# Optimization experiments

Measured on AMD Instinct MI355X. Metric: run time of the kernel, lower is better.

Reference implementation:

```python
import jax, jax.numpy as jnp
import numpy as np

N = 50000
F = 128
E = 800000
HOP = 3
ALPHA = 0.2  # leaky relu slope


def setup_inputs() -> dict:
    key = jax.random.key(0)
    ks = jax.random.split(key, 6)
    x = jax.random.normal(ks[0], (N, F), dtype=jnp.float32)
    h0 = jax.random.normal(ks[1], (N, F), dtype=jnp.float32)
    edge_index = jax.random.randint(ks[2], (2, E), 0, N, dtype=jnp.int32)
    edge_weight = jax.random.uniform(ks[3], (E,), dtype=jnp.float32)
    # xavier-uniform-ish params
    lim_w = float(np.sqrt(6.0 / (F + F)))
    W_att = jax.random.uniform(ks[4], (F, F), dtype=jnp.float32, minval=-lim_w, maxval=lim_w)
    lim_a = 1.414 * float(np.sqrt(6.0 / (2 * F + 1)))
    a = jax.random.uniform(ks[5], (2 * F, 1), dtype=jnp.float32, minval=-lim_a, maxval=lim_a)
    temp = jnp.zeros((4,), dtype=jnp.float32)
    return {"x": x, "h0": h0, "edge_index": edge_index, "edge_weight": edge_weight,
            "W_att": W_att, "a": a, "temp": temp}


def _segment_softmax(e, rows, num_segments):
    m = jax.ops.segment_max(e, rows, num_segments=num_segments)
    m = jnp.where(jnp.isfinite(m), m, 0.0)  # guard empty rows
    ex = jnp.exp(e - m[rows])
    s = jax.ops.segment_sum(ex, rows, num_segments=num_segments)
    s = jnp.where(s > 0, s, 1.0)
    return ex / s[rows]


def reference(x, h0, edge_index, edge_weight, W_att, a, temp):
    rows, cols = edge_index[0], edge_index[1]
    # --- attention (edge-wise, never materializing dense NxN e) ---
    feat = x @ W_att                       # [N, F]
    f1 = (feat @ a[:F]).squeeze(-1)        # [N]
    f2 = (feat @ a[F:]).squeeze(-1)        # [N]
    e = f1[rows] + f2[cols]                # e[i,j] at edges
    e = jnp.where(e > 0, e, ALPHA * e)     # leaky relu
    att = _segment_softmax(e, rows, N)     # sparse row softmax values
    P = 0.5 * att
    # --- lifting bases ---
    coe = jax.nn.sigmoid(temp)
    rowsum = jax.ops.segment_sum(edge_weight * P, rows, num_segments=N)  # [N]
    update = x
    feat_prime = None
    for step in range(HOP):
        # sparse mm: U @ update
        update = jax.ops.segment_sum(att[:, None] * update[cols], rows, num_segments=N)
        feat_even = coe[0] * x + update
        feat_odd = update - feat_even * rowsum[:, None]
        feat_prime = feat_odd if step == 0 else coe[2] * feat_prime + (1.0 - coe[2]) * feat_odd
    return feat_prime
```

## Files before the change

kernel.cpp:

```cpp
#include <hip/hip_runtime.h>
#include <hip/hip_fp16.h>

#define NN 50000
#define FF 128
#define EE 800000
#define ALPHA 0.2f
#define ESHIFT 4.0f

#define NBINS 196
#define CAPB 5120
#define EPB 2048
#define NWIN 784
#define WCAP 1600

__global__ void k_w(const float* __restrict__ W, const float* __restrict__ a,
                    float* __restrict__ w12) {
    int k = threadIdx.x;
    float s1 = 0.f, s2 = 0.f;
    const float* wr = W + k * FF;
    for (int j = 0; j < FF; ++j) {
        float w = wr[j];
        s1 += w * a[j];
        s2 += w * a[FF + j];
    }
    w12[k] = s1;
    w12[FF + k] = s2;
}

__global__ void k_f(const float* __restrict__ x, const float* __restrict__ w12,
                    float* __restrict__ f1, float* __restrict__ f2,
                    __half* __restrict__ xh) {
    int gid = blockIdx.x * blockDim.x + threadIdx.x;
    int node = gid >> 6;
    int lane = threadIdx.x & 63;
    if (node >= NN) return;
    float2 xv = ((const float2*)(x + (size_t)node * FF))[lane];
    ((__half2*)(xh + (size_t)node * FF))[lane] = __float22half2_rn(xv);
    float2 w1 = ((const float2*)w12)[lane];
    float2 w2 = ((const float2*)(w12 + FF))[lane];
    float s1 = xv.x * w1.x + xv.y * w1.y;
    float s2 = xv.x * w2.x + xv.y * w2.y;
#pragma unroll
    for (int o = 32; o > 0; o >>= 1) {
        s1 += __shfl_down(s1, o);
        s2 += __shfl_down(s2, o);
    }
    if (lane == 0) { f1[node] = s1; f2[node] = s2; }
}

__global__ void k_bin(const int* __restrict__ rows, const int* __restrict__ cols,
                      const float* __restrict__ ew, const float* __restrict__ f1,
                      const float* __restrict__ f2, int* __restrict__ bin_fill,
                      int2* __restrict__ binbuf) {
    __shared__ int cnt[NBINS];
    __shared__ int gbase[NBINS];
    int tid = threadIdx.x;
    if (tid < NBINS) cnt[tid] = 0;
    __syncthreads();
    int e0 = blockIdx.x * EPB;
    int rk[8], bn[8], rc[8], pay[8];
    bool vl[8];
#pragma unroll
    for (int k = 0; k < 8; ++k) {
        int e = e0 + k * 256 + tid;
        vl[k] = e < EE;
        if (vl[k]) {
            int r = rows[e], c = cols[e];
            float v = f1[r] + f2[c];
            v = v > 0.f ? v : ALPHA * v;
            float ex = __expf(v - ESHIFT);
            union { int i; __half2 h; } p;
            p.h = __floats2half2_rn(ex, ew[e] * ex);
            pay[k] = p.i;
            rc[k] = (r << 16) | c;
            bn[k] = r >> 8;
            rk[k] = atomicAdd(&cnt[bn[k]], 1);
        }
    }
    __syncthreads();
    if (tid < NBINS) {
        int c0 = cnt[tid];
        gbase[tid] = c0 ? atomicAdd(&bin_fill[tid], c0) : 0;
    }
    __syncthreads();
#pragma unroll
    for (int k = 0; k < 8; ++k) {
        if (vl[k]) {
            int pos = gbase[bn[k]] + rk[k];
            if (pos < CAPB) binbuf[(size_t)bn[k] * CAPB + pos] = make_int2(rc[k], pay[k]);
        }
    }
}

__global__ void k_csr(const int* __restrict__ bin_fill, const int2* __restrict__ binbuf,
                      int2* __restrict__ csr, int2* __restrict__ rowinfo) {
    __shared__ int lfill[64];
    __shared__ int pbase[65];
    __shared__ int cursor[64];
    int tid = threadIdx.x;
    int w = blockIdx.x;
    int bin = w >> 2, q = w & 3;
    int cnt = bin_fill[bin];
    if (cnt > CAPB) cnt = CAPB;
    if (tid < 64) lfill[tid] = 0;
    __syncthreads();
    const int2* bb = binbuf + (size_t)bin * CAPB;
    for (int i = tid; i < cnt; i += 256) {
        int rl = (bb[i].x >> 16) & 0xFF;
        if ((rl >> 6) == q) atomicAdd(&lfill[rl & 63], 1);
    }
    __syncthreads();
    if (tid < 64) {
        int pc = (lfill[tid] + 1) & ~1;
        int s = pc;
#pragma unroll
        for (int o = 1; o < 64; o <<= 1) {
            int t = __shfl_up(s, o);
            if (tid >= o) s += t;
        }
        pbase[tid + 1] = s;
        if (tid == 0) pbase[0] = 0;
    }
    __syncthreads();
    int wbase = w * WCAP;
    if (tid < 64) cursor[tid] = wbase + pbase[tid];
    __syncthreads();
    for (int i = tid; i < cnt; i += 256) {
        int2 e = bb[i];
        int rl = (e.x >> 16) & 0xFF;
        if ((rl >> 6) == q) {
            int p = atomicAdd(&cursor[rl & 63], 1);
            csr[p] = make_int2(e.x & 0xFFFF, e.y);
        }
    }
    __syncthreads();
    if (tid < 64) {
        int r = (bin << 8) + (q << 6) + tid;
        if (r < NN) {
            int beg = wbase + pbase[tid];
            int dreal = lfill[tid];
            int dpad = (dreal + 1) & ~1;
            if (dreal & 1) csr[beg + dreal] = make_int2(0, 0);
            rowinfo[r] = make_int2(beg, dpad);
        }
    }
}

__global__ void k_hop(const float* __restrict__ x, const __half* __restrict__ uin,
                      __half* __restrict__ uout, const int2* __restrict__ rowinfo,
                      const int2* __restrict__ csr, const float* __restrict__ temp,
                      __half* __restrict__ S, float* __restrict__ out, int step) {
    int wave = threadIdx.x >> 6;
    int lane = threadIdx.x & 63;
    int r = __builtin_amdgcn_readfirstlane(blockIdx.x * 4 + wave);
    if (r >= NN) return;
    int2 ri = rowinfo[r];
    const unsigned long long* bk = (const unsigned long long*)(csr + ri.x);
    int d = ri.y;
    float ax = 0.f, ay = 0.f, se = 0.f, sw = 0.f;
    int j = 0;
    for (; j + 8 <= d; j += 8) {
        unsigned long long b[8];
        __half2 h[8];
#pragma unroll
        for (int t = 0; t < 8; ++t) b[t] = __builtin_nontemporal_load(bk + j + t);
#pragma unroll
        for (int t = 0; t < 8; ++t) {
            int col = (int)(unsigned)(b[t] & 0xFFFFFFFFull);
            h[t] = ((const __half2*)(uin + (size_t)col * FF))[lane];
        }
#pragma unroll
        for (int t = 0; t < 8; ++t) {
            union { unsigned u; __half2 h2; } p;
            p.u = (unsigned)(b[t] >> 32);
            float2 ee = __half22float2(p.h2);
            float2 u = __half22float2(h[t]);
            ax += ee.x * u.x;
            ay += ee.x * u.y;
            se += ee.x;
            sw += ee.y;
        }
    }
    for (; j < d; ++j) {
        unsigned long long b = __builtin_nontemporal_load(bk + j);
        int col = (int)(unsigned)(b & 0xFFFFFFFFull);
        __half2 hv = ((const __half2*)(uin + (size_t)col * FF))[lane];
        union { unsigned u; __half2 h2; } p;
        p.u = (unsigned)(b >> 32);
        float2 ee = __half22float2(p.h2);
        float2 u = __half22float2(hv);
        ax += ee.x * u.x;
        ay += ee.x * u.y;
        se += ee.x;
        sw += ee.y;
    }
    float inv = se > 0.f ? 1.f / se : 0.f;
    ax *= inv;
    ay *= inv;
    float c2 = 1.f / (1.f + __expf(-temp[2]));
    __half2* Sr = (__half2*)(S + (size_t)r * FF);
    if (step == 0) {
        ((__half2*)(uout + (size_t)r * FF))[lane] = __float22half2_rn(make_float2(ax, ay));
        float w0 = c2 * c2;
        Sr[lane] = __float22half2_rn(make_float2(w0 * ax, w0 * ay));
    } else if (step == 1) {
        ((__half2*)(uout + (size_t)r * FF))[lane] = __float22half2_rn(make_float2(ax, ay));
        float w1 = c2 * (1.f - c2);
        float2 sv = __half22float2(Sr[lane]);
        Sr[lane] = __float22half2_rn(make_float2(sv.x + w1 * ax, sv.y + w1 * ay));
    } else {
        float rs = 0.5f * sw * inv;
        float coe0 = 1.f / (1.f + __expf(-temp[0]));
        float w2 = 1.f - c2;
        float2 sv = __half22float2(Sr[lane]);
        float2 xv = ((const float2*)(x + (size_t)r * FF))[lane];
        float k1 = 1.f - rs;
        float k2 = coe0 * rs;
        ((float2*)(out + (size_t)r * FF))[lane] =
            make_float2(k1 * (sv.x + w2 * ax) - k2 * xv.x,
                        k1 * (sv.y + w2 * ay) - k2 * xv.y);
    }
}

extern "C" void kernel_launch(void* const* d_in, const int* in_sizes, int n_in,
                              void* d_out, int out_size, void* d_ws, size_t ws_size,
                              hipStream_t stream) {
    const float* x = (const float*)d_in[0];
    const int* eidx = (const int*)d_in[2];
    const int* rows = eidx;
    const int* cols = eidx + EE;
    const float* ew = (const float*)d_in[3];
    const float* W = (const float*)d_in[4];
    const float* a = (const float*)d_in[5];
    const float* temp = (const float*)d_in[6];
    float* out = (float*)d_out;

    float* ws = (float*)d_ws;
    int* bin_fill = (int*)ws;
    float* w12 = ws + 256;
    float* f1 = ws + 512;
    float* f2 = f1 + NN;
    int2* rowinfo = (int2*)(f2 + NN);
    int2* csr = rowinfo + NN;
    __half* xh = (__half*)(csr + (size_t)NWIN * WCAP);
    __half* uh0 = xh + (size_t)NN * FF;
    __half* Sb = uh0 + (size_t)NN * FF;
    int2* binbuf = (int2*)Sb;
    __half* uh1 = xh;

    hipMemsetAsync(bin_fill, 0, NBINS * sizeof(int), stream);

    k_w<<<1, 128, 0, stream>>>(W, a, w12);
    k_f<<<(NN + 3) / 4, 256, 0, stream>>>(x, w12, f1, f2, xh);
    k_bin<<<(EE + EPB - 1) / EPB, 256, 0, stream>>>(rows, cols, ew, f1, f2, bin_fill, binbuf);
    k_csr<<<NWIN, 256, 0, stream>>>(bin_fill, binbuf, csr, rowinfo);
    k_hop<<<(NN + 3) / 4, 256, 0, stream>>>(x, xh, uh0, rowinfo, csr, temp, Sb, out, 0);
    k_hop<<<(NN + 3) / 4, 256, 0, stream>>>(x, uh0, uh1, rowinfo, csr, temp, Sb, out, 1);
    k_hop<<<(NN + 3) / 4, 256, 0, stream>>>(x, uh1, nullptr, rowinfo, csr, temp, Sb, out, 2);
}
```

Measured before the change: 247.6 us.

## Split hop SpMM rows into feature quarters with edge-parallel sub-waves

Each row of the sparse aggregation is now spread over four blocks, one per 32-feature quarter. Within a wave, four 16-lane groups each handle a different edge, and their partial sums are combined with cross-lane shuffles. CSR rows are padded to multiples of four so every edge group stays aligned. The goal is more waves in flight and more independent gathers to hide gather latency. The cost is four times as many reads of the CSR edge list, narrower 64-byte gathers, extra padding edges and reduction shuffles.

```diff
diff --git a/kernel.cpp b/kernel.cpp
--- a/kernel.cpp
+++ b/kernel.cpp
@@ -111,7 +111,7 @@
     }
     __syncthreads();
     if (tid < 64) {
-        int pc = (lfill[tid] + 1) & ~1;
+        int pc = (lfill[tid] + 3) & ~3;
         int s = pc;
 #pragma unroll
         for (int o = 1; o < 64; o <<= 1) {
@@ -139,8 +139,8 @@
         if (r < NN) {
             int beg = wbase + pbase[tid];
             int dreal = lfill[tid];
-            int dpad = (dreal + 1) & ~1;
-            if (dreal & 1) csr[beg + dreal] = make_int2(0, 0);
+            int dpad = (dreal + 3) & ~3;
+            for (int p = dreal; p < dpad; ++p) csr[beg + p] = make_int2(0, 0);
             rowinfo[r] = make_int2(beg, dpad);
         }
     }
@@ -152,73 +152,86 @@
                       __half* __restrict__ S, float* __restrict__ out, int step) {
     int wave = threadIdx.x >> 6;
     int lane = threadIdx.x & 63;
-    int r = __builtin_amdgcn_readfirstlane(blockIdx.x * 4 + wave);
+    int b = blockIdx.x;
+    int q = b & 3;
+    int r = __builtin_amdgcn_readfirstlane((b >> 2) * 4 + wave);
     if (r >= NN) return;
+    int sub = lane >> 4;
+    int fl = lane & 15;
     int2 ri = rowinfo[r];
     const unsigned long long* bk = (const unsigned long long*)(csr + ri.x);
     int d = ri.y;
+    const __half* ubase = uin + q * 32 + fl * 2;
     float ax = 0.f, ay = 0.f, se = 0.f, sw = 0.f;
     int j = 0;
     for (; j + 8 <= d; j += 8) {
-        unsigned long long b[8];
-        __half2 h[8];
-#pragma unroll
-        for (int t = 0; t < 8; ++t) b[t] = __builtin_nontemporal_load(bk + j + t);
-#pragma unroll
-        for (int t = 0; t < 8; ++t) {
-            int col = (int)(unsigned)(b[t] & 0xFFFFFFFFull);
-            h[t] = ((const __half2*)(uin + (size_t)col * FF))[lane];
-        }
-#pragma unroll
-        for (int t = 0; t < 8; ++t) {
-            union { unsigned u; __half2 h2; } p;
-            p.u = (unsigned)(b[t] >> 32);
-            float2 ee = __half22float2(p.h2);
-            float2 u = __half22float2(h[t]);
-            ax += ee.x * u.x;
-            ay += ee.x * u.y;
-            se += ee.x;
-            sw += ee.y;
-        }
-    }
-    for (; j < d; ++j) {
-        unsigned long long b = __builtin_nontemporal_load(bk + j);
-        int col = (int)(unsigned)(b & 0xFFFFFFFFull);
-        __half2 hv = ((const __half2*)(uin + (size_t)col * FF))[lane];
-        union { unsigned u; __half2 h2; } p;
-        p.u = (unsigned)(b >> 32);
-        float2 ee = __half22float2(p.h2);
-        float2 u = __half22float2(hv);
-        ax += ee.x * u.x;
-        ay += ee.x * u.y;
-        se += ee.x;
-        sw += ee.y;
-    }
+        unsigned long long b0 = __builtin_nontemporal_load(bk + j + sub);
+        unsigned long long b1 = __builtin_nontemporal_load(bk + j + 4 + sub);
+        int c0 = (int)(unsigned)(b0 & 0xFFFFFFFFull);
+        int c1 = (int)(unsigned)(b1 & 0xFFFFFFFFull);
+        __half2 h0 = *(const __half2*)(ubase + (size_t)c0 * FF);
+        __half2 h1 = *(const __half2*)(ubase + (size_t)c1 * FF);
+        union { unsigned u; __half2 h2; } p0, p1;
+        p0.u = (unsigned)(b0 >> 32);
+        p1.u = (unsigned)(b1 >> 32);
+        float2 e0 = __half22float2(p0.h2);
+        float2 e1 = __half22float2(p1.h2);
+        float2 u0 = __half22float2(h0);
+        float2 u1 = __half22float2(h1);
+        ax += e0.x * u0.x + e1.x * u1.x;
+        ay += e0.x * u0.y + e1.x * u1.y;
+        se += e0.x + e1.x;
+        sw += e0.y + e1.y;
+    }
+    for (; j < d; j += 4) {
+        unsigned long long b0 = __builtin_nontemporal_load(bk + j + sub);
+        int c0 = (int)(unsigned)(b0 & 0xFFFFFFFFull);
+        __half2 h0 = *(const __half2*)(ubase + (size_t)c0 * FF);
+        union { unsigned u; __half2 h2; } p0;
+        p0.u = (unsigned)(b0 >> 32);
+        float2 e0 = __half22float2(p0.h2);
+        float2 u0 = __half22float2(h0);
+        ax += e0.x * u0.x;
+        ay += e0.x * u0.y;
+        se += e0.x;
+        sw += e0.y;
+    }
+    ax += __shfl_xor(ax, 16); ax += __shfl_xor(ax, 32);
+    ay += __shfl_xor(ay, 16); ay += __shfl_xor(ay, 32);
+    se += __shfl_xor(se, 16); se += __shfl_xor(se, 32);
+    sw += __shfl_xor(sw, 16); sw += __shfl_xor(sw, 32);
     float inv = se > 0.f ? 1.f / se : 0.f;
     ax *= inv;
     ay *= inv;
     float c2 = 1.f / (1.f + __expf(-temp[2]));
-    __half2* Sr = (__half2*)(S + (size_t)r * FF);
+    __half2* Sr = (__half2*)(S + (size_t)r * FF + q * 32);
+    __half2* Ur = (__half2*)(uout + (size_t)r * FF + q * 32);
     if (step == 0) {
-        ((__half2*)(uout + (size_t)r * FF))[lane] = __float22half2_rn(make_float2(ax, ay));
-        float w0 = c2 * c2;
-        Sr[lane] = __float22half2_rn(make_float2(w0 * ax, w0 * ay));
+        if (sub == 0) Ur[fl] = __floats2half2_rn(ax, ay);
+        else if (sub == 1) {
+            float w0 = c2 * c2;
+            Sr[fl] = __floats2half2_rn(w0 * ax, w0 * ay);
+        }
     } else if (step == 1) {
-        ((__half2*)(uout + (size_t)r * FF))[lane] = __float22half2_rn(make_float2(ax, ay));
-        float w1 = c2 * (1.f - c2);
-        float2 sv = __half22float2(Sr[lane]);
-        Sr[lane] = __float22half2_rn(make_float2(sv.x + w1 * ax, sv.y + w1 * ay));
+        if (sub == 0) Ur[fl] = __floats2half2_rn(ax, ay);
+        else if (sub == 1) {
+            float w1 = c2 * (1.f - c2);
+            float2 sv = __half22float2(Sr[fl]);
+            Sr[fl] = __floats2half2_rn(sv.x + w1 * ax, sv.y + w1 * ay);
+        }
     } else {
-        float rs = 0.5f * sw * inv;
-        float coe0 = 1.f / (1.f + __expf(-temp[0]));
-        float w2 = 1.f - c2;
-        float2 sv = __half22float2(Sr[lane]);
-        float2 xv = ((const float2*)(x + (size_t)r * FF))[lane];
-        float k1 = 1.f - rs;
-        float k2 = coe0 * rs;
-        ((float2*)(out + (size_t)r * FF))[lane] =
-            make_float2(k1 * (sv.x + w2 * ax) - k2 * xv.x,
-                        k1 * (sv.y + w2 * ay) - k2 * xv.y);
+        if (sub == 0) {
+            float rs = 0.5f * sw * inv;
+            float coe0 = 1.f / (1.f + __expf(-temp[0]));
+            float w2 = 1.f - c2;
+            float2 sv = __half22float2(Sr[fl]);
+            float2 xv = ((const float2*)(x + (size_t)r * FF + q * 32))[fl];
+            float k1 = 1.f - rs;
+            float k2 = coe0 * rs;
+            ((float2*)(out + (size_t)r * FF + q * 32))[fl] =
+                make_float2(k1 * (sv.x + w2 * ax) - k2 * xv.x,
+                            k1 * (sv.y + w2 * ay) - k2 * xv.y);
+        }
     }
 }
 
@@ -254,7 +267,7 @@
     k_f<<<(NN + 3) / 4, 256, 0, stream>>>(x, w12, f1, f2, xh);
     k_bin<<<(EE + EPB - 1) / EPB, 256, 0, stream>>>(rows, cols, ew, f1, f2, bin_fill, binbuf);
     k_csr<<<NWIN, 256, 0, stream>>>(bin_fill, binbuf, csr, rowinfo);
-    k_hop<<<(NN + 3) / 4, 256, 0, stream>>>(x, xh, uh0, rowinfo, csr, temp, Sb, out, 0);
-    k_hop<<<(NN + 3) / 4, 256, 0, stream>>>(x, uh0, uh1, rowinfo, csr, temp, Sb, out, 1);
-    k_hop<<<(NN + 3) / 4, 256, 0, stream>>>(x, uh1, nullptr, rowinfo, csr, temp, Sb, out, 2);
-}
+    k_hop<<<NN, 256, 0, stream>>>(x, xh, uh0, rowinfo, csr, temp, Sb, out, 0);
+    k_hop<<<NN, 256, 0, stream>>>(x, uh0, uh1, rowinfo, csr, temp, Sb, out, 1);
+    k_hop<<<NN, 256, 0, stream>>>(x, uh1, nullptr, rowinfo, csr, temp, Sb, out, 2);
+}
```

Result: slower. 454.0 us (+83.3%).

## Precompute row softmax sums in CSR build and software-pipeline hop gathers

Applied to the files above, without the earlier changes.

Pads each CSR row to a multiple of 8 so the hop kernel needs no scalar tail loop. It also moves the per-row attention sum and weighted rowsum into k_csr, storing them in a new rowmeta array, and double-buffers the 8-wide gather loop so the next batch's loads overlap the current accumulation. This removes per-hop reductions and loop tails and hides gather latency. In exchange it adds padded zero-weight gathers, more registers per lane and a serial per-row sum in k_csr.

```diff
diff --git a/kernel.cpp b/kernel.cpp
--- a/kernel.cpp
+++ b/kernel.cpp
@@ -93,7 +93,8 @@
 }
 
 __global__ void k_csr(const int* __restrict__ bin_fill, const int2* __restrict__ binbuf,
-                      int2* __restrict__ csr, int2* __restrict__ rowinfo) {
+                      int2* __restrict__ csr, int2* __restrict__ rowinfo,
+                      float2* __restrict__ rowmeta) {
     __shared__ int lfill[64];
     __shared__ int pbase[65];
     __shared__ int cursor[64];
@@ -111,7 +112,7 @@
     }
     __syncthreads();
     if (tid < 64) {
-        int pc = (lfill[tid] + 1) & ~1;
+        int pc = (lfill[tid] + 7) & ~7;
         int s = pc;
 #pragma unroll
         for (int o = 1; o < 64; o <<= 1) {
@@ -139,64 +140,81 @@
         if (r < NN) {
             int beg = wbase + pbase[tid];
             int dreal = lfill[tid];
-            int dpad = (dreal + 1) & ~1;
-            if (dreal & 1) csr[beg + dreal] = make_int2(0, 0);
+            int dpad = (dreal + 7) & ~7;
+            for (int p = dreal; p < dpad; ++p) csr[beg + p] = make_int2(0, 0);
+            float se = 0.f, sw = 0.f;
+            for (int i = 0; i < dreal; ++i) {
+                union { int i32; __half2 h; } pp;
+                pp.i32 = csr[beg + i].y;
+                float2 e2 = __half22float2(pp.h);
+                se += e2.x;
+                sw += e2.y;
+            }
+            float inv = se > 0.f ? 1.f / se : 0.f;
             rowinfo[r] = make_int2(beg, dpad);
+            rowmeta[r] = make_float2(inv, 0.5f * sw * inv);
         }
     }
 }
 
 __global__ void k_hop(const float* __restrict__ x, const __half* __restrict__ uin,
                       __half* __restrict__ uout, const int2* __restrict__ rowinfo,
-                      const int2* __restrict__ csr, const float* __restrict__ temp,
-                      __half* __restrict__ S, float* __restrict__ out, int step) {
+                      const float2* __restrict__ rowmeta, const int2* __restrict__ csr,
+                      const float* __restrict__ temp, __half* __restrict__ S,
+                      float* __restrict__ out, int step) {
     int wave = threadIdx.x >> 6;
     int lane = threadIdx.x & 63;
     int r = __builtin_amdgcn_readfirstlane(blockIdx.x * 4 + wave);
     if (r >= NN) return;
     int2 ri = rowinfo[r];
+    float2 mt = rowmeta[r];
     const unsigned long long* bk = (const unsigned long long*)(csr + ri.x);
     int d = ri.y;
-    float ax = 0.f, ay = 0.f, se = 0.f, sw = 0.f;
-    int j = 0;
-    for (; j + 8 <= d; j += 8) {
+    float ax = 0.f, ay = 0.f;
+    if (d > 0) {
         unsigned long long b[8];
         __half2 h[8];
 #pragma unroll
-        for (int t = 0; t < 8; ++t) b[t] = __builtin_nontemporal_load(bk + j + t);
+        for (int t = 0; t < 8; ++t) b[t] = __builtin_nontemporal_load(bk + t);
 #pragma unroll
         for (int t = 0; t < 8; ++t) {
-            int col = (int)(unsigned)(b[t] & 0xFFFFFFFFull);
+            int col = (int)(unsigned)b[t];
             h[t] = ((const __half2*)(uin + (size_t)col * FF))[lane];
         }
+        for (int j = 8; j + 8 <= d; j += 8) {
+            unsigned long long b2[8];
+            __half2 h2[8];
+#pragma unroll
+            for (int t = 0; t < 8; ++t) b2[t] = __builtin_nontemporal_load(bk + j + t);
+#pragma unroll
+            for (int t = 0; t < 8; ++t) {
+                int col = (int)(unsigned)b2[t];
+                h2[t] = ((const __half2*)(uin + (size_t)col * FF))[lane];
+            }
+#pragma unroll
+            for (int t = 0; t < 8; ++t) {
+                union { unsigned u; __half2 h2v; } p;
+                p.u = (unsigned)(b[t] >> 32);
+                float att = __half2float(__low2half(p.h2v));
+                float2 u = __half22float2(h[t]);
+                ax += att * u.x;
+                ay += att * u.y;
+            }
+#pragma unroll
+            for (int t = 0; t < 8; ++t) { b[t] = b2[t]; h[t] = h2[t]; }
+        }
 #pragma unroll
         for (int t = 0; t < 8; ++t) {
-            union { unsigned u; __half2 h2; } p;
+            union { unsigned u; __half2 h2v; } p;
             p.u = (unsigned)(b[t] >> 32);
-            float2 ee = __half22float2(p.h2);
+            float att = __half2float(__low2half(p.h2v));
             float2 u = __half22float2(h[t]);
-            ax += ee.x * u.x;
-            ay += ee.x * u.y;
-            se += ee.x;
-            sw += ee.y;
-        }
-    }
-    for (; j < d; ++j) {
-        unsigned long long b = __builtin_nontemporal_load(bk + j);
-        int col = (int)(unsigned)(b & 0xFFFFFFFFull);
-        __half2 hv = ((const __half2*)(uin + (size_t)col * FF))[lane];
-        union { unsigned u; __half2 h2; } p;
-        p.u = (unsigned)(b >> 32);
-        float2 ee = __half22float2(p.h2);
-        float2 u = __half22float2(hv);
-        ax += ee.x * u.x;
-        ay += ee.x * u.y;
-        se += ee.x;
-        sw += ee.y;
-    }
-    float inv = se > 0.f ? 1.f / se : 0.f;
-    ax *= inv;
-    ay *= inv;
+            ax += att * u.x;
+            ay += att * u.y;
+        }
+    }
+    ax *= mt.x;
+    ay *= mt.x;
     float c2 = 1.f / (1.f + __expf(-temp[2]));
     __half2* Sr = (__half2*)(S + (size_t)r * FF);
     if (step == 0) {
@@ -209,7 +227,7 @@
         float2 sv = __half22float2(Sr[lane]);
         Sr[lane] = __float22half2_rn(make_float2(sv.x + w1 * ax, sv.y + w1 * ay));
     } else {
-        float rs = 0.5f * sw * inv;
+        float rs = mt.y;
         float coe0 = 1.f / (1.f + __expf(-temp[0]));
         float w2 = 1.f - c2;
         float2 sv = __half22float2(Sr[lane]);
@@ -241,7 +259,8 @@
     float* f1 = ws + 512;
     float* f2 = f1 + NN;
     int2* rowinfo = (int2*)(f2 + NN);
-    int2* csr = rowinfo + NN;
+    float2* rowmeta = (float2*)(rowinfo + NN);
+    int2* csr = (int2*)(rowmeta + NN);
     __half* xh = (__half*)(csr + (size_t)NWIN * WCAP);
     __half* uh0 = xh + (size_t)NN * FF;
     __half* Sb = uh0 + (size_t)NN * FF;
@@ -253,8 +272,8 @@
     k_w<<<1, 128, 0, stream>>>(W, a, w12);
     k_f<<<(NN + 3) / 4, 256, 0, stream>>>(x, w12, f1, f2, xh);
     k_bin<<<(EE + EPB - 1) / EPB, 256, 0, stream>>>(rows, cols, ew, f1, f2, bin_fill, binbuf);
-    k_csr<<<NWIN, 256, 0, stream>>>(bin_fill, binbuf, csr, rowinfo);
-    k_hop<<<(NN + 3) / 4, 256, 0, stream>>>(x, xh, uh0, rowinfo, csr, temp, Sb, out, 0);
-    k_hop<<<(NN + 3) / 4, 256, 0, stream>>>(x, uh0, uh1, rowinfo, csr, temp, Sb, out, 1);
-    k_hop<<<(NN + 3) / 4, 256, 0, stream>>>(x, uh1, nullptr, rowinfo, csr, temp, Sb, out, 2);
-}
+    k_csr<<<NWIN, 256, 0, stream>>>(bin_fill, binbuf, csr, rowinfo, rowmeta);
+    k_hop<<<(NN + 3) / 4, 256, 0, stream>>>(x, xh, uh0, rowinfo, rowmeta, csr, temp, Sb, out, 0);
+    k_hop<<<(NN + 3) / 4, 256, 0, stream>>>(x, uh0, uh1, rowinfo, rowmeta, csr, temp, Sb, out, 1);
+    k_hop<<<(NN + 3) / 4, 256, 0, stream>>>(x, uh1, nullptr, rowinfo, rowmeta, csr, temp, Sb, out, 2);
+}
```

Measured after the change: 248.3 us. Within noise of the previous version (+0.3%).
